# Kernel optimization log

Hardware: AMD Instinct MI355X
Metric: run time of the kernel (lower is better)

The kernel has to match this reference:

```python
import jax, jax.numpy as jnp
import numpy as np

POOL = 7
NUM_ROIS = 256
SCALE = 1.0 / 16.0  # feature-map stride
H, W, C = 128, 128, 1024
STRIDE = 16


def setup_inputs() -> dict:
    key = jax.random.key(0)
    k_img, k_wh, k_xy = jax.random.split(key, 3)
    img = jax.random.normal(k_img, (1, H, W, C), dtype=jnp.float32)
    # ROIs in image-pixel units (x, y, w, h); w,h >= 16 so crop >= 1 feature cell
    max_px = H * STRIDE  # 2048
    wh = jax.random.uniform(k_wh, (1, NUM_ROIS, 2), minval=16.0, maxval=max_px * 0.5)
    xy = jax.random.uniform(k_xy, (1, NUM_ROIS, 2), minval=0.0, maxval=1.0) * (max_px - wh)
    rois = jnp.concatenate([xy, wh], axis=-1).astype(jnp.float32)
    return {"img": img, "rois": rois}


def _pool_one_roi(img0, roi):
    # img0: (H, W, C); roi: (4,) = (x, y, w, h) in pixels.
    # Original: int cast of scaled coords, crop img[y:y+h, x:x+w],
    # then TF1 bilinear resize (align_corners=False, src = i * in/out).
    c = (roi * SCALE).astype(jnp.int32)  # truncation == floor for positive coords
    x0, y0, w, h = c[0], c[1], c[2], c[3]
    i = jnp.arange(POOL, dtype=jnp.float32)
    # source coords within the cropped section
    sy = i * (h.astype(jnp.float32) / POOL)
    sx = i * (w.astype(jnp.float32) / POOL)
    fy = jnp.floor(sy)
    fx = jnp.floor(sx)
    ty = sy - fy  # (P,) lerp weights
    tx = sx - fx
    y_lo = fy.astype(jnp.int32)
    x_lo = fx.astype(jnp.int32)
    y_hi = jnp.minimum(y_lo + 1, jnp.maximum(h - 1, 0))  # clamp at section edge
    x_hi = jnp.minimum(x_lo + 1, jnp.maximum(w - 1, 0))
    gy0 = jnp.clip(y0 + y_lo, 0, H - 1)
    gy1 = jnp.clip(y0 + y_hi, 0, H - 1)
    gx0 = jnp.clip(x0 + x_lo, 0, W - 1)
    gx1 = jnp.clip(x0 + x_hi, 0, W - 1)
    v00 = img0[gy0[:, None], gx0[None, :]]  # (P, P, C)
    v01 = img0[gy0[:, None], gx1[None, :]]
    v10 = img0[gy1[:, None], gx0[None, :]]
    v11 = img0[gy1[:, None], gx1[None, :]]
    top = v00 + tx[None, :, None] * (v01 - v00)
    bot = v10 + tx[None, :, None] * (v11 - v10)
    return top + ty[:, None, None] * (bot - top)  # (P, P, C)


def reference(img, rois):
    img0 = img[0]  # (H, W, C)
    pooled = jax.vmap(lambda r: _pool_one_roi(img0, r))(rois[0])  # (NR, P, P, C)
    return pooled[None]  # (1, num_rois, pool, pool, C)
```

## Files before the change

kernel.cpp:

```cpp
#include <hip/hip_runtime.h>


#define IMG_H 128
#define IMG_W 128
#define IMG_C 1024
#define POOLK 7
#define NROIS 256

typedef float vfloat4 __attribute__((ext_vector_type(4)));

__global__ __launch_bounds__(256) void roi_pool_kernel(
    const float* __restrict__ img,
    const float* __restrict__ rois,
    float* __restrict__ out) {
  const int iy = blockIdx.x;
  const int r  = blockIdx.y;

  const vfloat4 roi = *(const vfloat4*)(rois + (size_t)r * 4);

  const int x0 = (int)(roi.x * 0.0625f);
  const int y0 = (int)(roi.y * 0.0625f);
  const int w  = (int)(roi.z * 0.0625f);
  const int h  = (int)(roi.w * 0.0625f);

  const float sy = (float)iy * ((float)h / 7.0f);
  const float fy = floorf(sy);
  const float ty = sy - fy;
  const int y_lo = (int)fy;
  const int y_hi = min(y_lo + 1, max(h - 1, 0));
  const int gy0 = min(max(y0 + y_lo, 0), IMG_H - 1);
  const int gy1 = min(max(y0 + y_hi, 0), IMG_H - 1);

  const int c = threadIdx.x * 4;
  const float* row0 = img + (size_t)gy0 * (IMG_W * IMG_C) + c;
  const float* row1 = img + (size_t)gy1 * (IMG_W * IMG_C) + c;
  float* orow = out + (((size_t)r * POOLK + iy) * POOLK) * IMG_C + c;

  const float step_x = (float)w / 7.0f;
  const int xmax = max(w - 1, 0);

#pragma unroll
  for (int ix = 0; ix < POOLK; ++ix) {
    const float sx = (float)ix * step_x;
    const float fx = floorf(sx);
    const float tx = sx - fx;
    const int x_lo = (int)fx;
    const int x_hi = min(x_lo + 1, xmax);
    const int gx0 = min(max(x0 + x_lo, 0), IMG_W - 1);
    const int gx1 = min(max(x0 + x_hi, 0), IMG_W - 1);

    const vfloat4 v00 = *(const vfloat4*)(row0 + (size_t)gx0 * IMG_C);
    const vfloat4 v01 = *(const vfloat4*)(row0 + (size_t)gx1 * IMG_C);
    const vfloat4 v10 = *(const vfloat4*)(row1 + (size_t)gx0 * IMG_C);
    const vfloat4 v11 = *(const vfloat4*)(row1 + (size_t)gx1 * IMG_C);

    const vfloat4 top = v00 + tx * (v01 - v00);
    const vfloat4 bot = v10 + tx * (v11 - v10);
    const vfloat4 o   = top + ty * (bot - top);

    *(vfloat4*)(orow + (size_t)ix * IMG_C) = o;
  }
}

extern "C" void kernel_launch(void* const* d_in, const int* in_sizes, int n_in,
                              void* d_out, int out_size, void* d_ws, size_t ws_size,
                              hipStream_t stream) {
  const float* img  = (const float*)d_in[0];
  const float* rois = (const float*)d_in[1];
  float* out = (float*)d_out;

  dim3 grid(POOLK, NROIS);
  dim3 block(256);
  roi_pool_kernel<<<grid, block, 0, stream>>>(img, rois, out);
}
```

Baseline: 120.2 us.

## Split channels into slices mapped per XCD for L2 locality, nontemporal stores

Changes the work decomposition from (pool row, ROI) blocks covering all channels to blocks that each handle a 32-channel slice for all 49 cells of one ROI. Block indices are arranged so each XCD processes one channel slice across all ROIs at a time, which keeps that slice of the image resident in the XCD's L2. Output is written with nontemporal stores so it does not evict image data, and the ROI scalars are made wave-uniform. In exchange each thread now does only 16-byte loads spread over many cells, there are more blocks with 15 of 64 cell slots idle, and the mapping relies on the hardware dispatching blocks to XCDs round-robin.

```diff
diff --git a/kernel.cpp b/kernel.cpp
--- a/kernel.cpp
+++ b/kernel.cpp
@@ -7,58 +7,79 @@
 #define POOLK 7
 #define NROIS 256
 
+#define SLICE_C 32
+#define NSLICE (IMG_C / SLICE_C)
+#define NXCD 8
+#define NPHASE (NSLICE / NXCD)
+#define NBLK (NROIS * NSLICE)
+
 typedef float vfloat4 __attribute__((ext_vector_type(4)));
 
-__global__ __launch_bounds__(256) void roi_pool_kernel(
+__global__ __launch_bounds__(256, 8) void roi_pool_kernel(
     const float* __restrict__ img,
     const float* __restrict__ rois,
     float* __restrict__ out) {
-  const int iy = blockIdx.x;
-  const int r  = blockIdx.y;
+  const int b = (int)blockIdx.x;
+  const int x8 = b & 7;
+  const int k = b >> 3;
+  const int r = k & (NROIS - 1);
+  const int phase = k >> 8;
+  const int slice = phase * NXCD + x8;
+  const int cbase = slice * SLICE_C;
 
   const vfloat4 roi = *(const vfloat4*)(rois + (size_t)r * 4);
+  const int x0 = __builtin_amdgcn_readfirstlane((int)(roi.x * 0.0625f));
+  const int y0 = __builtin_amdgcn_readfirstlane((int)(roi.y * 0.0625f));
+  const int w  = __builtin_amdgcn_readfirstlane((int)(roi.z * 0.0625f));
+  const int h  = __builtin_amdgcn_readfirstlane((int)(roi.w * 0.0625f));
 
-  const int x0 = (int)(roi.x * 0.0625f);
-  const int y0 = (int)(roi.y * 0.0625f);
-  const int w  = (int)(roi.z * 0.0625f);
-  const int h  = (int)(roi.w * 0.0625f);
-
-  const float sy = (float)iy * ((float)h / 7.0f);
-  const float fy = floorf(sy);
-  const float ty = sy - fy;
-  const int y_lo = (int)fy;
-  const int y_hi = min(y_lo + 1, max(h - 1, 0));
-  const int gy0 = min(max(y0 + y_lo, 0), IMG_H - 1);
-  const int gy1 = min(max(y0 + y_hi, 0), IMG_H - 1);
-
-  const int c = threadIdx.x * 4;
-  const float* row0 = img + (size_t)gy0 * (IMG_W * IMG_C) + c;
-  const float* row1 = img + (size_t)gy1 * (IMG_W * IMG_C) + c;
-  float* orow = out + (((size_t)r * POOLK + iy) * POOLK) * IMG_C + c;
-
-  const float step_x = (float)w / 7.0f;
+  const float step_y = (float)h * (1.0f / 7.0f);
+  const float step_x = (float)w * (1.0f / 7.0f);
+  const int ymax = max(h - 1, 0);
   const int xmax = max(w - 1, 0);
 
+  const int lane  = (int)threadIdx.x & 7;
+  const int cell0 = (int)threadIdx.x >> 3;
+  const int coff  = cbase + lane * 4;
+
 #pragma unroll
-  for (int ix = 0; ix < POOLK; ++ix) {
-    const float sx = (float)ix * step_x;
-    const float fx = floorf(sx);
-    const float tx = sx - fx;
-    const int x_lo = (int)fx;
-    const int x_hi = min(x_lo + 1, xmax);
-    const int gx0 = min(max(x0 + x_lo, 0), IMG_W - 1);
-    const int gx1 = min(max(x0 + x_hi, 0), IMG_W - 1);
+  for (int half = 0; half < 2; ++half) {
+    const int cell = cell0 + half * 32;
+    if (cell < POOLK * POOLK) {
+      const int iy = cell / POOLK;
+      const int ix = cell - iy * POOLK;
 
-    const vfloat4 v00 = *(const vfloat4*)(row0 + (size_t)gx0 * IMG_C);
-    const vfloat4 v01 = *(const vfloat4*)(row0 + (size_t)gx1 * IMG_C);
-    const vfloat4 v10 = *(const vfloat4*)(row1 + (size_t)gx0 * IMG_C);
-    const vfloat4 v11 = *(const vfloat4*)(row1 + (size_t)gx1 * IMG_C);
+      const float sy = (float)iy * step_y;
+      const float fy = floorf(sy);
+      const float ty = sy - fy;
+      const int y_lo = (int)fy;
+      const int y_hi = min(y_lo + 1, ymax);
+      const int gy0 = min(max(y0 + y_lo, 0), IMG_H - 1);
+      const int gy1 = min(max(y0 + y_hi, 0), IMG_H - 1);
 
-    const vfloat4 top = v00 + tx * (v01 - v00);
-    const vfloat4 bot = v10 + tx * (v11 - v10);
-    const vfloat4 o   = top + ty * (bot - top);
+      const float sx = (float)ix * step_x;
+      const float fx = floorf(sx);
+      const float tx = sx - fx;
+      const int x_lo = (int)fx;
+      const int x_hi = min(x_lo + 1, xmax);
+      const int gx0 = min(max(x0 + x_lo, 0), IMG_W - 1);
+      const int gx1 = min(max(x0 + x_hi, 0), IMG_W - 1);
 
-    *(vfloat4*)(orow + (size_t)ix * IMG_C) = o;
+      const float* r0 = img + (size_t)(gy0 * IMG_W) * IMG_C + coff;
+      const float* r1 = img + (size_t)(gy1 * IMG_W) * IMG_C + coff;
+
+      const vfloat4 v00 = *(const vfloat4*)(r0 + (size_t)gx0 * IMG_C);
+      const vfloat4 v01 = *(const vfloat4*)(r0 + (size_t)gx1 * IMG_C);
+      const vfloat4 v10 = *(const vfloat4*)(r1 + (size_t)gx0 * IMG_C);
+      const vfloat4 v11 = *(const vfloat4*)(r1 + (size_t)gx1 * IMG_C);
+
+      const vfloat4 top = v00 + tx * (v01 - v00);
+      const vfloat4 bot = v10 + tx * (v11 - v10);
+      const vfloat4 o   = top + ty * (bot - top);
+
+      float* op = out + (((size_t)r * POOLK + iy) * POOLK + ix) * IMG_C + coff;
+      __builtin_nontemporal_store(o, (vfloat4*)op);
+    }
   }
 }
 
@@ -69,7 +90,7 @@
   const float* rois = (const float*)d_in[1];
   float* out = (float*)d_out;
 
-  dim3 grid(POOLK, NROIS);
+  dim3 grid(NBLK);
   dim3 block(256);
   roi_pool_kernel<<<grid, block, 0, stream>>>(img, rois, out);
 }
```

Result: slower. 127.2 us (+5.9%).
